# Optimization experiments

Measured on AMD Instinct MI355X. Metric: run time of the kernel, lower is better.

Reference implementation:

```python
import jax, jax.numpy as jnp
import numpy as np

IOU_THRESHOLD = 0.5


def setup_inputs() -> dict:
    key = jax.random.key(0)
    k1, k2, k3 = jax.random.split(key, 3)
    B, N = 4, 8192
    # valid boxes: top-left in [0,200), width/height in [1,51)
    xy = jax.random.uniform(k1, (B, N, 2), dtype=jnp.float32) * 200.0
    wh = jax.random.uniform(k2, (B, N, 2), dtype=jnp.float32) * 50.0 + 1.0
    boxes = jnp.concatenate([xy, xy + wh], axis=-1)  # [B,N,4] (x1,y1,x2,y2)
    scores = jax.random.uniform(k3, (B, N), dtype=jnp.float32)
    return {"boxes": boxes, "scores": scores}


def _soft_nms_single(boxes, scores):
    # boxes: [N,4], scores: [N]
    x1, y1, x2, y2 = boxes[:, 0], boxes[:, 1], boxes[:, 2], boxes[:, 3]
    inter_w = jnp.maximum(0.0, jnp.minimum(x2[:, None], x2[None, :]) - jnp.maximum(x1[:, None], x1[None, :]))
    inter_h = jnp.maximum(0.0, jnp.minimum(y2[:, None], y2[None, :]) - jnp.maximum(y1[:, None], y1[None, :]))
    inter = inter_w * inter_h  # [N,N]
    area = (x2 - x1) * (y2 - y1)  # [N]
    union = area[:, None] + area[None, :] - inter
    iou = inter / union  # [N,N]
    weight = jnp.exp(-iou / IOU_THRESHOLD)  # [N,N]
    adjusted = weight @ scores  # [N] : adjusted_scores[i] = sum_j w[i,j]*s[j]
    w = jax.nn.softmax(adjusted, axis=0)  # [N]
    return w @ boxes  # [4]


def reference(boxes, scores):
    return jax.vmap(_soft_nms_single)(boxes, scores)  # [B,4]
```

## Files before the change

kernel.cpp:

```cpp
#include <hip/hip_runtime.h>
#include <hip/hip_bf16.h>

#define BATCH   4
#define NBOX    8192
#define BLOCK   256
#define TSZ     256
#define NT      (NBOX / TSZ)
#define NPAIRS  (NT * (NT + 1) / 2)
#define NBINS   2048
#define SUBS    8
#define SUBSZ   (NBOX / SUBS)
#define STH     512

__device__ __forceinline__ float bf2f(unsigned short u) {
    union { unsigned int i; float f; } c;
    c.i = ((unsigned int)u) << 16;
    return c.f;
}

__device__ __forceinline__ bool box_plausible(float x1, float y1, float x2, float y2) {
    bool ok = (x1 == x1) && (y1 == y1) && (x2 == x2) && (y2 == y2);
    ok = ok && fabsf(x1) < 1e4f && fabsf(y1) < 1e4f && fabsf(x2) < 1e4f && fabsf(y2) < 1e4f;
    ok = ok && x1 >= -1.0f && x1 <= 300.0f && y1 >= -1.0f && y1 <= 300.0f;
    const float w = x2 - x1, h = y2 - y1;
    ok = ok && w >= -0.1f && w <= 80.0f && h >= -0.1f && h <= 80.0f;
    return ok;
}

__device__ __forceinline__ bool wave_probe_is_f32(const void* boxes_raw) {
    const int lane = threadIdx.x & 63;
    const float* bf = (const float*)boxes_raw;
    const bool okf = box_plausible(bf[lane * 4 + 0], bf[lane * 4 + 1],
                                   bf[lane * 4 + 2], bf[lane * 4 + 3]);
    const unsigned short* bh = (const unsigned short*)boxes_raw;
    const bool okh = box_plausible(bf2f(bh[lane * 4 + 0]), bf2f(bh[lane * 4 + 1]),
                                   bf2f(bh[lane * 4 + 2]), bf2f(bh[lane * 4 + 3]));
    const unsigned long long mf = __ballot(okf);
    const unsigned long long mh = __ballot(okh);
    return __popcll(mf) >= __popcll(mh);
}

__device__ __forceinline__ float4 load_box(const void* boxes_raw, size_t idx, bool isf32) {
    if (isf32) {
        return reinterpret_cast<const float4*>(boxes_raw)[idx];
    } else {
        const ushort4 u = reinterpret_cast<const ushort4*>(boxes_raw)[idx];
        return make_float4(bf2f(u.x), bf2f(u.y), bf2f(u.z), bf2f(u.w));
    }
}

__device__ __forceinline__ float load_score(const void* scores_raw, size_t idx, bool isf32) {
    return isf32 ? ((const float*)scores_raw)[idx]
                 : bf2f(((const unsigned short*)scores_raw)[idx]);
}

__device__ __forceinline__ int key_bin(float v) {
    const int bb = (int)(v * 8.0f);
    return min(NBINS - 1, max(0, bb));
}

#define CEXP (-2.8853900817779268f)

__device__ __forceinline__ float pair_weight(
    float ix1, float iy1, float ix2, float iy2, float iarea,
    const float4& bj, float jarea)
{
    float w = fminf(ix2, bj.z) - fmaxf(ix1, bj.x);
    float h = fminf(iy2, bj.w) - fmaxf(iy1, bj.y);
    w = fmaxf(w, 0.0f);
    h = fmaxf(h, 0.0f);
    const float inter = w * h;
    const float uni   = iarea + jarea - inter;
    const float arg   = (CEXP * inter) * __builtin_amdgcn_rcpf(uni);
    return __builtin_amdgcn_exp2f(arg);
}

__global__ __launch_bounds__(STH) void sort_kernel(
    const void* __restrict__ boxes_raw, const void* __restrict__ scores_raw,
    float4* __restrict__ sboxes, float* __restrict__ sscores,
    float* __restrict__ adj, float* __restrict__ adjc,
    float* __restrict__ minx1c, float* __restrict__ maxx2c,
    int* __restrict__ pairlist, int* __restrict__ count)
{
    __shared__ int hist[NBINS];
    __shared__ int bmin[NBINS];
    __shared__ int hist2[NBINS];
    __shared__ int wsum[STH / 64];
    __shared__ float sminT[NT], smaxT[NT];
    __shared__ int scnt;

    const int b    = blockIdx.x / SUBS;
    const int sub  = blockIdx.x % SUBS;
    const int tid  = threadIdx.x;
    const int lane = tid & 63;
    const int wv   = tid >> 6;
    const bool isf32 = wave_probe_is_f32(boxes_raw);
    const size_t base = (size_t)b * NBOX;

#pragma unroll
    for (int i = 0; i < NBINS / STH; i++) {
        hist[i * STH + tid]  = 0;
        bmin[i * STH + tid]  = 0x7f800000;
        hist2[i * STH + tid] = 0;
    }
    if (tid == 0) scnt = 0;
    {
        const size_t z = (size_t)blockIdx.x * 1024;
        adj[z + tid] = 0.0f;
        adj[z + STH + tid] = 0.0f;
        adjc[z + tid] = 0.0f;
        adjc[z + STH + tid] = 0.0f;
    }
    __syncthreads();

    const int sublim = sub * SUBSZ;
#pragma unroll
    for (int k = 0; k < NBOX / STH; k++) {
        const int i = k * STH + tid;
        const float4 bx = load_box(boxes_raw, base + i, isf32);
        const int bin = key_bin(bx.z);
        atomicAdd(&hist[bin], 1);
        atomicMin(&bmin[bin], __float_as_int(bx.x));
        if (i < sublim) atomicAdd(&hist2[bin], 1);
    }
    __syncthreads();

    {
        int tot[4], cum[4];
        int run = 0;
#pragma unroll
        for (int i = 0; i < 4; i++) {
            tot[i] = hist[tid * 4 + i];
            run += tot[i]; cum[i] = run;
        }
        int v = run;
#pragma unroll
        for (int d = 1; d < 64; d <<= 1) {
            const int u = __shfl_up(v, d);
            if (lane >= d) v += u;
        }
        if (lane == 63) wsum[wv] = v;
        __syncthreads();
        int wb = 0;
        for (int w = 0; w < wv; w++) wb += wsum[w];
        const int tb = wb + v - run;
#pragma unroll
        for (int i = 0; i < 4; i++) {
            const int bin = tid * 4 + i;
            const int e = tb + cum[i] - tot[i];
            const int m = hist2[bin];
            hist[bin]  = e;
            hist2[bin] = e + m;
        }
    }
    __syncthreads();

    if (tid < NT) {
        int p = tid * TSZ;
        int lo = 0, hi = NBINS - 1;
        while (lo < hi) { const int mid = (lo + hi + 1) >> 1;
                          if (hist[mid] <= p) lo = mid; else hi = mid - 1; }
        const int Bf = lo;
        p = tid * TSZ + TSZ - 1;
        lo = 0; hi = NBINS - 1;
        while (lo < hi) { const int mid = (lo + hi + 1) >> 1;
                          if (hist[mid] <= p) lo = mid; else hi = mid - 1; }
        const int Bl = lo;
        float mn = 3.4e38f;
        for (int q = Bf; q <= Bl; q++) mn = fminf(mn, __int_as_float(bmin[q]));
        const float mx = (float)(Bl + 1) * 0.125f;
        sminT[tid] = mn; smaxT[tid] = mx;
        if (sub == 0) {
            minx1c[b * NT + tid] = mn;
            maxx2c[b * NT + tid] = mx;
        }
    }
    __syncthreads();

    if (sub == 0) {
        for (int q = tid; q < NPAIRS; q += STH) {
            int p = q, it = 0;
            while (p >= NT - it) { p -= NT - it; it++; }
            const int jt = it + p;
            const bool live = !((smaxT[it] < sminT[jt]) || (smaxT[jt] < sminT[it]));
            if (live) {
                const int idx = atomicAdd(&scnt, 1);
                pairlist[b * NPAIRS + idx] = (it << 8) | jt;
            }
        }
    }

#pragma unroll
    for (int k = 0; k < SUBSZ / STH; k++) {
        const int i = sub * SUBSZ + k * STH + tid;
        const float4 bx = load_box(boxes_raw, base + i, isf32);
        const float  sc = load_score(scores_raw, base + i, isf32);
        const int pos = atomicAdd(&hist2[key_bin(bx.z)], 1);
        sboxes[base + pos]  = bx;
        sscores[base + pos] = sc;
    }

    __syncthreads();
    if (sub == 0 && tid == 0) count[b] = scnt;
}

__global__ __launch_bounds__(TSZ) void perm_kernel(
    const float4* __restrict__ sboxes, const float* __restrict__ sscores,
    float4* __restrict__ cboxes, float2* __restrict__ cas,
    int* __restrict__ cinv,
    float* __restrict__ cgmin)
{
    __shared__ float sx1[TSZ];
    const int tile = blockIdx.x;
    const size_t gbase = (size_t)tile * TSZ;
    const int tid = threadIdx.x;

    const float4 u = sboxes[gbase + tid];
    const float sc = sscores[gbase + tid];
    sx1[tid] = u.x;
    __syncthreads();

    int rank = 0;
#pragma unroll 8
    for (int j = 0; j < TSZ; j++) {
        const float v = sx1[j];
        rank += (v < u.x || (v == u.x && j < tid)) ? 1 : 0;
    }

    cboxes[gbase + rank] = u;
    cas[gbase + rank] = make_float2((u.z - u.x) * (u.w - u.y), sc);
    cinv[gbase + tid] = rank;
    if ((rank & 63) == 0) cgmin[tile * 4 + (rank >> 6)] = u.x;
}

__global__ __launch_bounds__(BLOCK, 8) void soft_nms_adj_kernel(
    const float4* __restrict__ sboxes,
    const float* __restrict__ sscores,
    const float4* __restrict__ cboxes,
    const float2* __restrict__ cas,
    const float* __restrict__ cgmin,
    const int* __restrict__ pairlist,
    const int* __restrict__ count,
    float* __restrict__ adj,
    float* __restrict__ adjc)
{
    __shared__ float4 sbox[TSZ];
    __shared__ float2 sas[TSZ];
    __shared__ float  srow[4][TSZ];

    const int bid = blockIdx.x;
    const int b   = bid / NPAIRS;
    const int p   = bid % NPAIRS;
    if (p >= count[b]) return;
    const int pr = pairlist[b * NPAIRS + p];
    const int it = pr >> 8, jt = pr & 255;

    const int tid  = threadIdx.x;
    const int lane = tid & 63;
    const int wv   = tid >> 6;
    const size_t base = (size_t)b * NBOX;

    float ws;
    {
        const int jg = jt * TSZ + tid;
        const float4 uj = cboxes[base + jg];
        sbox[tid] = uj;
        const float2 asv = cas[base + jg];
        sas[tid]  = asv;
        float w0 = asv.y;
#pragma unroll
        for (int off = 32; off > 0; off >>= 1) w0 += __shfl_xor(w0, off);
        ws = w0;
    }

    float rx1[4], ry1[4], rx2[4], ry2[4], rar[4], rsc[4];
#pragma unroll
    for (int k = 0; k < 4; k++) {
        const int ig = it * TSZ + k * 64 + lane;
        const float4 ui = sboxes[base + ig];
        rx1[k] = ui.x; ry1[k] = ui.y; rx2[k] = ui.z; ry2[k] = ui.w;
        rar[k] = (ui.z - ui.x) * (ui.w - ui.y);
        rsc[k] = sscores[base + ig];
    }

    int kstart = 0;
    if (it != jt) {
        const float cg = cgmin[(b * NT + jt) * 4 + wv];
#pragma unroll
        for (int k = 0; k < 4; k++) {
            const float gmax = __shfl(rx2[k], 63) + 0.125f;
            if (kstart == k && gmax < cg) kstart = k + 1;
        }
    }
    float ccorr = 0.0f;
    if (kstart > 0) {
#pragma unroll
        for (int k = 0; k < 4; k++) {
            if (k < kstart) {
                float gs = rsc[k];
#pragma unroll
                for (int off = 32; off > 0; off >>= 1) gs += __shfl_xor(gs, off);
                ccorr += gs;
            }
        }
    }

    __syncthreads();

    float accr[4];
#pragma unroll
    for (int k = 0; k < 4; k++) accr[k] = (k < kstart) ? ws : 0.0f;

    const int wvbase = wv * 64;

    if (it == jt) {
#pragma unroll 2
        for (int t = 0; t < 64; t++) {
            const int idx = wvbase + ((lane + t) & 63);
            const float4 bj = sbox[idx];
            const float2 as = sas[idx];
#pragma unroll
            for (int k = 0; k < 4; k++) {
                const float e = pair_weight(rx1[k], ry1[k], rx2[k], ry2[k], rar[k], bj, as.x);
                accr[k] = fmaf(e, as.y, accr[k]);
            }
        }
    } else {
#define OFFD_LOOP(KS)                                                          \
        {                                                                      \
            float accc = ccorr;                                                \
            _Pragma("unroll 2")                                                \
            for (int t = 0; t < 64; t++) {                                     \
                const int idx = wvbase + ((lane + t) & 63);                    \
                const float4 bj = sbox[idx];                                   \
                const float2 as = sas[idx];                                    \
                float c = 0.0f;                                                \
                _Pragma("unroll")                                              \
                for (int k = KS; k < 4; ++k) {                                 \
                    const float e = pair_weight(rx1[k], ry1[k], rx2[k], ry2[k],\
                                                rar[k], bj, as.x);             \
                    accr[k] = fmaf(e, as.y, accr[k]);                          \
                    c = fmaf(e, rsc[k], c);                                    \
                }                                                              \
                accc += __shfl(c, (lane - t) & 63);                            \
            }                                                                  \
            atomicAdd(&adjc[base + jt * TSZ + wvbase + lane], accc);           \
        }
        switch (kstart) {
            case 0: OFFD_LOOP(0); break;
            case 1: OFFD_LOOP(1); break;
            case 2: OFFD_LOOP(2); break;
            case 3: OFFD_LOOP(3); break;
            default:
                atomicAdd(&adjc[base + jt * TSZ + wvbase + lane], ccorr);
                break;
        }
#undef OFFD_LOOP
    }

#pragma unroll
    for (int k = 0; k < 4; k++) srow[wv][k * 64 + lane] = accr[k];
    __syncthreads();
    {
        const float rs = srow[0][tid] + srow[1][tid] + srow[2][tid] + srow[3][tid];
        atomicAdd(&adj[base + it * TSZ + tid], rs);
    }
}

#define FBLK 1024
__global__ __launch_bounds__(FBLK) void soft_nms_finish_kernel(
    const float4* __restrict__ sboxes,
    const float* __restrict__ sscores,
    const float* __restrict__ adj,
    const float* __restrict__ adjc,
    const int* __restrict__ cinv,
    const float* __restrict__ minx1c, const float* __restrict__ maxx2c,
    const void* __restrict__ boxes_raw,
    void* __restrict__ out)
{
    constexpr int K  = NBOX / FBLK;
    constexpr int NW = FBLK / 64;
    __shared__ float sminx[NT], smaxx[NT], ssumT[NT], scorr[NT];
    __shared__ float smax_[NW];
    __shared__ float sred[NW][5];

    const int b    = blockIdx.x;
    const int tid  = threadIdx.x;
    const int lane = tid & 63;
    const int wv   = tid >> 6;
    const size_t base = (size_t)b * NBOX;

    const bool isf32 = wave_probe_is_f32(boxes_raw);

    if (tid < NT) {
        sminx[tid] = minx1c[b * NT + tid];
        smaxx[tid] = maxx2c[b * NT + tid];
    }
#pragma unroll
    for (int tt = 0; tt < 2; tt++) {
        const int T = wv * 2 + tt;
        float sm = 0.0f;
#pragma unroll
        for (int q = 0; q < 4; q++) sm += sscores[base + T * TSZ + q * 64 + lane];
#pragma unroll
        for (int off = 32; off > 0; off >>= 1) sm += __shfl_down(sm, off);
        if (lane == 0) ssumT[T] = sm;
    }
    __syncthreads();
    if (tid < NT) {
        float c = 0.0f;
        for (int T2 = 0; T2 < NT; T2++) {
            const bool skip = (smaxx[tid] < sminx[T2]) || (smaxx[T2] < sminx[tid]);
            if (skip) c += ssumT[T2];
        }
        scorr[tid] = c;
    }
    __syncthreads();

    float av[K];
    float m = -3.4e38f;
#pragma unroll
    for (int k = 0; k < K; k++) {
        const int r = k * FBLK + tid;
        const int pos = cinv[base + r];
        av[k] = adj[base + r] + adjc[base + (r & ~255) + pos] + scorr[r >> 8];
        m = fmaxf(m, av[k]);
    }
#pragma unroll
    for (int off = 32; off > 0; off >>= 1)
        m = fmaxf(m, __shfl_down(m, off));
    if (lane == 0) smax_[wv] = m;
    __syncthreads();
    float M = smax_[0];
#pragma unroll
    for (int w = 1; w < NW; w++) M = fmaxf(M, smax_[w]);

    const float L2E = 1.4426950408889634f;
    float es = 0.0f, s0 = 0.0f, s1 = 0.0f, s2 = 0.0f, s3 = 0.0f;
#pragma unroll
    for (int k = 0; k < K; k++) {
        const float e = __builtin_amdgcn_exp2f((av[k] - M) * L2E);
        const float4 u = sboxes[base + k * FBLK + tid];
        es += e;
        s0 += e * u.x;
        s1 += e * u.y;
        s2 += e * u.z;
        s3 += e * u.w;
    }
#pragma unroll
    for (int off = 32; off > 0; off >>= 1) {
        es += __shfl_down(es, off);
        s0 += __shfl_down(s0, off);
        s1 += __shfl_down(s1, off);
        s2 += __shfl_down(s2, off);
        s3 += __shfl_down(s3, off);
    }
    if (lane == 0) {
        sred[wv][0] = es; sred[wv][1] = s0; sred[wv][2] = s1;
        sred[wv][3] = s2; sred[wv][4] = s3;
    }
    __syncthreads();
    if (tid == 0) {
        float ES = 0.0f, o[4] = {0.0f, 0.0f, 0.0f, 0.0f};
#pragma unroll
        for (int w = 0; w < NW; w++) {
            ES   += sred[w][0];
            o[0] += sred[w][1];
            o[1] += sred[w][2];
            o[2] += sred[w][3];
            o[3] += sred[w][4];
        }
        const float inv = 1.0f / ES;
        if (isf32) {
            float* of = (float*)out;
            for (int c = 0; c < 4; c++) of[b * 4 + c] = o[c] * inv;
        } else {
            __hip_bfloat16* oh = (__hip_bfloat16*)out;
            for (int c = 0; c < 4; c++) oh[b * 4 + c] = __float2bfloat16(o[c] * inv);
        }
    }
}

extern "C" void kernel_launch(void* const* d_in, const int* in_sizes, int n_in,
                              void* d_out, int out_size, void* d_ws, size_t ws_size,
                              hipStream_t stream) {
    const void* boxes_raw  = d_in[0];
    const void* scores_raw = d_in[1];

    char* w = (char*)d_ws;
    float4* sboxes   = (float4*)w;                 w += (size_t)BATCH * NBOX * 16;
    float4* cboxes   = (float4*)w;                 w += (size_t)BATCH * NBOX * 16;
    float2* cas      = (float2*)w;                 w += (size_t)BATCH * NBOX * 8;
    float*  sscores  = (float*)w;                  w += (size_t)BATCH * NBOX * 4;
    float*  adj      = (float*)w;                  w += (size_t)BATCH * NBOX * 4;
    float*  adjc     = (float*)w;                  w += (size_t)BATCH * NBOX * 4;
    int*    cinv     = (int*)w;                    w += (size_t)BATCH * NBOX * 4;
    float*  minx1c   = (float*)w;                  w += (size_t)BATCH * NT * 4;
    float*  maxx2c   = (float*)w;                  w += (size_t)BATCH * NT * 4;
    float*  cgmin    = (float*)w;                  w += (size_t)BATCH * NT * 4 * 4;
    int*    pairlist = (int*)w;                    w += (size_t)BATCH * NPAIRS * 4;
    int*    count    = (int*)w;

    sort_kernel<<<dim3(BATCH * SUBS), dim3(STH), 0, stream>>>(
        boxes_raw, scores_raw, sboxes, sscores, adj, adjc, minx1c, maxx2c, pairlist, count);
    perm_kernel<<<dim3(BATCH * NT), dim3(TSZ), 0, stream>>>(
        sboxes, sscores, cboxes, cas, cinv, cgmin);
    soft_nms_adj_kernel<<<dim3(BATCH * NPAIRS), dim3(BLOCK), 0, stream>>>(
        sboxes, sscores, cboxes, cas, cgmin, pairlist, count, adj, adjc);
    soft_nms_finish_kernel<<<dim3(BATCH), dim3(FBLK), 0, stream>>>(
        sboxes, sscores, adj, adjc, cinv, minx1c, maxx2c, boxes_raw, d_out);
}
```

Before: 140.7 us.

## Fold per-tile x1 sort into adjacency kernel and drop separate perm kernel

Measured after the change: 129.2 us. -8.1%, faster.

```diff
diff --git a/kernel.cpp b/kernel.cpp
--- a/kernel.cpp
+++ b/kernel.cpp
@@ -78,7 +78,7 @@
 __global__ __launch_bounds__(STH) void sort_kernel(
     const void* __restrict__ boxes_raw, const void* __restrict__ scores_raw,
     float4* __restrict__ sboxes, float* __restrict__ sscores,
-    float* __restrict__ adj, float* __restrict__ adjc,
+    float* __restrict__ adj,
     float* __restrict__ minx1c, float* __restrict__ maxx2c,
     int* __restrict__ pairlist, int* __restrict__ count)
 {
@@ -108,8 +108,6 @@
         const size_t z = (size_t)blockIdx.x * 1024;
         adj[z + tid] = 0.0f;
         adj[z + STH + tid] = 0.0f;
-        adjc[z + tid] = 0.0f;
-        adjc[z + STH + tid] = 0.0f;
     }
     __syncthreads();
 
@@ -204,49 +202,18 @@
     if (sub == 0 && tid == 0) count[b] = scnt;
 }
 
-__global__ __launch_bounds__(TSZ) void perm_kernel(
-    const float4* __restrict__ sboxes, const float* __restrict__ sscores,
-    float4* __restrict__ cboxes, float2* __restrict__ cas,
-    int* __restrict__ cinv,
-    float* __restrict__ cgmin)
-{
-    __shared__ float sx1[TSZ];
-    const int tile = blockIdx.x;
-    const size_t gbase = (size_t)tile * TSZ;
-    const int tid = threadIdx.x;
-
-    const float4 u = sboxes[gbase + tid];
-    const float sc = sscores[gbase + tid];
-    sx1[tid] = u.x;
-    __syncthreads();
-
-    int rank = 0;
-#pragma unroll 8
-    for (int j = 0; j < TSZ; j++) {
-        const float v = sx1[j];
-        rank += (v < u.x || (v == u.x && j < tid)) ? 1 : 0;
-    }
-
-    cboxes[gbase + rank] = u;
-    cas[gbase + rank] = make_float2((u.z - u.x) * (u.w - u.y), sc);
-    cinv[gbase + tid] = rank;
-    if ((rank & 63) == 0) cgmin[tile * 4 + (rank >> 6)] = u.x;
-}
-
-__global__ __launch_bounds__(BLOCK, 8) void soft_nms_adj_kernel(
+__global__ __launch_bounds__(BLOCK, 4) void soft_nms_adj_kernel(
     const float4* __restrict__ sboxes,
     const float* __restrict__ sscores,
-    const float4* __restrict__ cboxes,
-    const float2* __restrict__ cas,
-    const float* __restrict__ cgmin,
     const int* __restrict__ pairlist,
     const int* __restrict__ count,
-    float* __restrict__ adj,
-    float* __restrict__ adjc)
+    float* __restrict__ adj)
 {
     __shared__ float4 sbox[TSZ];
     __shared__ float2 sas[TSZ];
+    __shared__ int    sidx[TSZ];
     __shared__ float  srow[4][TSZ];
+    __shared__ float  cgminS[4];
 
     const int bid = blockIdx.x;
     const int b   = bid / NPAIRS;
@@ -260,20 +227,7 @@
     const int wv   = tid >> 6;
     const size_t base = (size_t)b * NBOX;
 
-    float ws;
-    {
-        const int jg = jt * TSZ + tid;
-        const float4 uj = cboxes[base + jg];
-        sbox[tid] = uj;
-        const float2 asv = cas[base + jg];
-        sas[tid]  = asv;
-        float w0 = asv.y;
-#pragma unroll
-        for (int off = 32; off > 0; off >>= 1) w0 += __shfl_xor(w0, off);
-        ws = w0;
-    }
-
-    float rx1[4], ry1[4], rx2[4], ry2[4], rar[4], rsc[4];
+    float rx1[4], ry1[4], rx2[4], ry2[4], rar[4], rsc[4], accr[4];
 #pragma unroll
     for (int k = 0; k < 4; k++) {
         const int ig = it * TSZ + k * 64 + lane;
@@ -281,39 +235,17 @@
         rx1[k] = ui.x; ry1[k] = ui.y; rx2[k] = ui.z; ry2[k] = ui.w;
         rar[k] = (ui.z - ui.x) * (ui.w - ui.y);
         rsc[k] = sscores[base + ig];
-    }
-
-    int kstart = 0;
-    if (it != jt) {
-        const float cg = cgmin[(b * NT + jt) * 4 + wv];
-#pragma unroll
-        for (int k = 0; k < 4; k++) {
-            const float gmax = __shfl(rx2[k], 63) + 0.125f;
-            if (kstart == k && gmax < cg) kstart = k + 1;
-        }
-    }
-    float ccorr = 0.0f;
-    if (kstart > 0) {
-#pragma unroll
-        for (int k = 0; k < 4; k++) {
-            if (k < kstart) {
-                float gs = rsc[k];
-#pragma unroll
-                for (int off = 32; off > 0; off >>= 1) gs += __shfl_xor(gs, off);
-                ccorr += gs;
-            }
-        }
-    }
-
-    __syncthreads();
-
-    float accr[4];
-#pragma unroll
-    for (int k = 0; k < 4; k++) accr[k] = (k < kstart) ? ws : 0.0f;
+        accr[k] = 0.0f;
+    }
 
     const int wvbase = wv * 64;
+    const float4 uj = sboxes[base + jt * TSZ + tid];
+    const float  jsc = sscores[base + jt * TSZ + tid];
 
     if (it == jt) {
+        sbox[tid] = uj;
+        sas[tid]  = make_float2((uj.z - uj.x) * (uj.w - uj.y), jsc);
+        __syncthreads();
 #pragma unroll 2
         for (int t = 0; t < 64; t++) {
             const int idx = wvbase + ((lane + t) & 63);
@@ -326,6 +258,50 @@
             }
         }
     } else {
+        float* skey = srow[0];
+        skey[tid] = uj.x;
+        __syncthreads();
+        int rank = 0;
+#pragma unroll 8
+        for (int j = 0; j < TSZ; j++) {
+            const float v = skey[j];
+            rank += (v < uj.x || (v == uj.x && j < tid)) ? 1 : 0;
+        }
+        __syncthreads();
+        sbox[rank] = uj;
+        sas[rank]  = make_float2((uj.z - uj.x) * (uj.w - uj.y), jsc);
+        sidx[rank] = tid;
+        if ((rank & 63) == 0) cgminS[rank >> 6] = uj.x;
+        __syncthreads();
+
+        float ws = sas[wvbase + lane].y;
+#pragma unroll
+        for (int off = 32; off > 0; off >>= 1) ws += __shfl_xor(ws, off);
+
+        const float cg = cgminS[wv];
+        int kstart = 0;
+#pragma unroll
+        for (int k = 0; k < 4; k++) {
+            const float gmax = __shfl(rx2[k], 63) + 0.125f;
+            if (kstart == k && gmax < cg) kstart = k + 1;
+        }
+        float ccorr = 0.0f;
+        if (kstart > 0) {
+#pragma unroll
+            for (int k = 0; k < 4; k++) {
+                if (k < kstart) {
+                    float gs = rsc[k];
+#pragma unroll
+                    for (int off = 32; off > 0; off >>= 1) gs += __shfl_xor(gs, off);
+                    ccorr += gs;
+                }
+            }
+        }
+#pragma unroll
+        for (int k = 0; k < 4; k++) accr[k] = (k < kstart) ? ws : 0.0f;
+
+        const int cj = sidx[wvbase + lane];
+
 #define OFFD_LOOP(KS)                                                          \
         {                                                                      \
             float accc = ccorr;                                                \
@@ -344,7 +320,7 @@
                 }                                                              \
                 accc += __shfl(c, (lane - t) & 63);                            \
             }                                                                  \
-            atomicAdd(&adjc[base + jt * TSZ + wvbase + lane], accc);           \
+            atomicAdd(&adj[base + jt * TSZ + cj], accc);                       \
         }
         switch (kstart) {
             case 0: OFFD_LOOP(0); break;
@@ -352,12 +328,13 @@
             case 2: OFFD_LOOP(2); break;
             case 3: OFFD_LOOP(3); break;
             default:
-                atomicAdd(&adjc[base + jt * TSZ + wvbase + lane], ccorr);
+                atomicAdd(&adj[base + jt * TSZ + cj], ccorr);
                 break;
         }
 #undef OFFD_LOOP
     }
 
+    __syncthreads();
 #pragma unroll
     for (int k = 0; k < 4; k++) srow[wv][k * 64 + lane] = accr[k];
     __syncthreads();
@@ -372,8 +349,6 @@
     const float4* __restrict__ sboxes,
     const float* __restrict__ sscores,
     const float* __restrict__ adj,
-    const float* __restrict__ adjc,
-    const int* __restrict__ cinv,
     const float* __restrict__ minx1c, const float* __restrict__ maxx2c,
     const void* __restrict__ boxes_raw,
     void* __restrict__ out)
@@ -422,8 +397,7 @@
 #pragma unroll
     for (int k = 0; k < K; k++) {
         const int r = k * FBLK + tid;
-        const int pos = cinv[base + r];
-        av[k] = adj[base + r] + adjc[base + (r & ~255) + pos] + scorr[r >> 8];
+        av[k] = adj[base + r] + scorr[r >> 8];
         m = fmaxf(m, av[k]);
     }
 #pragma unroll
@@ -489,24 +463,17 @@
 
     char* w = (char*)d_ws;
     float4* sboxes   = (float4*)w;                 w += (size_t)BATCH * NBOX * 16;
-    float4* cboxes   = (float4*)w;                 w += (size_t)BATCH * NBOX * 16;
-    float2* cas      = (float2*)w;                 w += (size_t)BATCH * NBOX * 8;
     float*  sscores  = (float*)w;                  w += (size_t)BATCH * NBOX * 4;
     float*  adj      = (float*)w;                  w += (size_t)BATCH * NBOX * 4;
-    float*  adjc     = (float*)w;                  w += (size_t)BATCH * NBOX * 4;
-    int*    cinv     = (int*)w;                    w += (size_t)BATCH * NBOX * 4;
     float*  minx1c   = (float*)w;                  w += (size_t)BATCH * NT * 4;
     float*  maxx2c   = (float*)w;                  w += (size_t)BATCH * NT * 4;
-    float*  cgmin    = (float*)w;                  w += (size_t)BATCH * NT * 4 * 4;
     int*    pairlist = (int*)w;                    w += (size_t)BATCH * NPAIRS * 4;
     int*    count    = (int*)w;
 
     sort_kernel<<<dim3(BATCH * SUBS), dim3(STH), 0, stream>>>(
-        boxes_raw, scores_raw, sboxes, sscores, adj, adjc, minx1c, maxx2c, pairlist, count);
-    perm_kernel<<<dim3(BATCH * NT), dim3(TSZ), 0, stream>>>(
-        sboxes, sscores, cboxes, cas, cinv, cgmin);
+        boxes_raw, scores_raw, sboxes, sscores, adj, minx1c, maxx2c, pairlist, count);
     soft_nms_adj_kernel<<<dim3(BATCH * NPAIRS), dim3(BLOCK), 0, stream>>>(
-        sboxes, sscores, cboxes, cas, cgmin, pairlist, count, adj, adjc);
+        sboxes, sscores, pairlist, count, adj);
     soft_nms_finish_kernel<<<dim3(BATCH), dim3(FBLK), 0, stream>>>(
-        sboxes, sscores, adj, adjc, cinv, minx1c, maxx2c, boxes_raw, d_out);
-}
+        sboxes, sscores, adj, minx1c, maxx2c, boxes_raw, d_out);
+}
```
